# Kernel optimization log

Measured on AMD Instinct MI355X. Metric: run time of the kernel, lower is better.

## Reference

```python
import jax, jax.numpy as jnp
import numpy as np

B, T, D = 4, 2048, 1024  # batch, seq, latent_dim == attn_dim
H = 16                   # n_heads
HS = D // H              # head_size = 64
FF = 4 * D               # ffn hidden
EPS = 1e-5


def layernorm(x, g, b):
    mu = jnp.mean(x, axis=-1, keepdims=True)
    var = jnp.mean(jnp.square(x - mu), axis=-1, keepdims=True)
    return (x - mu) * jax.lax.rsqrt(var + EPS) * g + b


def setup_inputs() -> dict:
    key = jax.random.key(0)
    ks = jax.random.split(key, 12)
    s = lambda fan_in: 1.0 / np.sqrt(fan_in)
    return {
        "x": jax.random.normal(ks[0], (B, T, D), dtype=jnp.float32),
        "ln1_g": jnp.ones((D,), jnp.float32),
        "ln1_b": jnp.zeros((D,), jnp.float32),
        "W_ap": jax.random.normal(ks[1], (D, D), jnp.float32) * s(D),
        "b_ap": jnp.zeros((D,), jnp.float32),
        "W_qkv": jax.random.normal(ks[2], (D, 3 * D), jnp.float32) * s(D),
        "b_qkv": jnp.zeros((3 * D,), jnp.float32),
        "W_proj": jax.random.normal(ks[3], (D, D), jnp.float32) * s(D),
        "b_proj": jnp.zeros((D,), jnp.float32),
        "ln2_g": jnp.ones((D,), jnp.float32),
        "ln2_b": jnp.zeros((D,), jnp.float32),
        "W1": jax.random.normal(ks[4], (D, FF), jnp.float32) * s(D),
        "b1": jnp.zeros((FF,), jnp.float32),
        "W2": jax.random.normal(ks[5], (FF, D), jnp.float32) * s(FF),
        "b2": jnp.zeros((D,), jnp.float32),
    }


def block_fwd(x, ln1_g, ln1_b, W_ap, b_ap, W_qkv, b_qkv, W_proj, b_proj,
              ln2_g, ln2_b, W1, b1, W2, b2):
    # --- self attention branch ---
    a = layernorm(x, ln1_g, ln1_b)
    a = a @ W_ap + b_ap                       # [B,T,D]
    qkv = a @ W_qkv + b_qkv                   # [B,T,3D]
    q, k, v = jnp.split(qkv, 3, axis=-1)
    q = q.reshape(B, T, H, HS).transpose(0, 2, 1, 3)  # [B,H,T,HS]
    k = k.reshape(B, T, H, HS).transpose(0, 2, 1, 3)
    v = v.reshape(B, T, H, HS).transpose(0, 2, 1, 3)
    scores = jnp.einsum('bhqd,bhkd->bhqk', q, k) * (1.0 / np.sqrt(HS))
    probs = jax.nn.softmax(scores, axis=-1)   # full [B,H,T,T], no causal mask (as in source)
    o = jnp.einsum('bhqk,bhkd->bhqd', probs, v)
    o = o.transpose(0, 2, 1, 3).reshape(B, T, D)
    o = o @ W_proj + b_proj
    h = x + o
    # --- ffn branch: GELU(LayerNorm(h)) -> Linear -> GELU -> Linear ---
    f = jax.nn.gelu(layernorm(h, ln2_g, ln2_b), approximate=False)
    f = jax.nn.gelu(f @ W1 + b1, approximate=False) @ W2 + b2
    return h + f


def reference(x, ln1_g, ln1_b, W_ap, b_ap, W_qkv, b_qkv, W_proj, b_proj,
              ln2_g, ln2_b, W1, b1, W2, b2):
    return block_fwd(x, ln1_g, ln1_b, W_ap, b_ap, W_qkv, b_qkv, W_proj, b_proj,
                     ln2_g, ln2_b, W1, b1, W2, b2)
```

## Files before the change

kernel.cpp:

```cpp
#include <hip/hip_runtime.h>
#include <hip/hip_bf16.h>
#include <math.h>


typedef unsigned short u16;
typedef __attribute__((ext_vector_type(8))) short s16x8;
typedef __attribute__((ext_vector_type(4))) float f32x4;

__device__ __forceinline__ u16 f2bf(float f) {
    unsigned u = __float_as_uint(f);
    u += 0x7fffu + ((u >> 16) & 1u);
    return (u16)(u >> 16);
}
__device__ __forceinline__ unsigned pkbf2(float a, float b) {
    float2 t; t.x = a; t.y = b;
    __hip_bfloat162 r = __float22bfloat162_rn(t);
    return *(unsigned*)&r;
}
__device__ __forceinline__ float bf2f(short s) {
    return __uint_as_float(((unsigned)(unsigned short)s) << 16);
}
__device__ __forceinline__ float gelu_f(float v) {
    float u = v * v;
    float x = v * fmaf(0.0356774081f, u, 0.7978845608f);
    float t = __builtin_amdgcn_exp2f(x * 2.885390082f);
    float th = fmaf(-2.0f, __builtin_amdgcn_rcpf(t + 1.0f), 1.0f);
    float hv = 0.5f * v;
    return fmaf(hv, th, hv);
}
__device__ __forceinline__ void glds16(const u16* g, u16* l) {
    __builtin_amdgcn_global_load_lds(
        (const __attribute__((address_space(1))) void*)g,
        (__attribute__((address_space(3))) void*)l, 16, 0, 0);
}
__device__ __forceinline__ void barfence() {
    __builtin_amdgcn_s_barrier();
    asm volatile("" ::: "memory");
}

__global__ __launch_bounds__(256) void transpose_f32_bf16(
    const float* __restrict__ in, u16* __restrict__ out, int K, int N) {
    __shared__ float t[32][33];
    int n0 = blockIdx.x * 32, k0 = blockIdx.y * 32;
    int c = threadIdx.x, r0 = threadIdx.y;
#pragma unroll
    for (int i = 0; i < 4; i++) {
        int r = r0 + i * 8;
        t[r][c] = in[(size_t)(k0 + r) * N + n0 + c];
    }
    __syncthreads();
#pragma unroll
    for (int i = 0; i < 4; i++) {
        int r = r0 + i * 8;
        out[(size_t)(n0 + r) * K + k0 + c] = f2bf(t[c][r]);
    }
}

template <bool GELU>
__global__ __launch_bounds__(256) void ln_kernel(
    const float* __restrict__ x, const float* __restrict__ g,
    const float* __restrict__ bt, u16* __restrict__ out) {
    const int D = 1024;
    int row = blockIdx.x;
    float4 v = reinterpret_cast<const float4*>(x + (size_t)row * D)[threadIdx.x];
    float s = v.x + v.y + v.z + v.w;
    float s2 = v.x * v.x + v.y * v.y + v.z * v.z + v.w * v.w;
#pragma unroll
    for (int off = 32; off > 0; off >>= 1) {
        s += __shfl_down(s, off);
        s2 += __shfl_down(s2, off);
    }
    __shared__ float red[8];
    int wid = threadIdx.x >> 6;
    if ((threadIdx.x & 63) == 0) { red[wid] = s; red[wid + 4] = s2; }
    __syncthreads();
    s = red[0] + red[1] + red[2] + red[3];
    s2 = red[4] + red[5] + red[6] + red[7];
    float mu = s * (1.0f / 1024.0f);
    float var = s2 * (1.0f / 1024.0f) - mu * mu;
    float rstd = rsqrtf(var + 1e-5f);
    float4 gg = reinterpret_cast<const float4*>(g)[threadIdx.x];
    float4 bb = reinterpret_cast<const float4*>(bt)[threadIdx.x];
    float o0 = (v.x - mu) * rstd * gg.x + bb.x;
    float o1 = (v.y - mu) * rstd * gg.y + bb.y;
    float o2 = (v.z - mu) * rstd * gg.z + bb.z;
    float o3 = (v.w - mu) * rstd * gg.w + bb.w;
    if (GELU) { o0 = gelu_f(o0); o1 = gelu_f(o1); o2 = gelu_f(o2); o3 = gelu_f(o3); }
    uint2 o;
    o.x = pkbf2(o0, o1); o.y = pkbf2(o2, o3);
    reinterpret_cast<uint2*>(out + (size_t)row * D)[threadIdx.x] = o;
}

template <int OUT_BF16, int ACT_GELU, int HAS_RES, int SPLIT_V>
__global__ __launch_bounds__(512, 2) void gemm_kernel(
    const u16* __restrict__ A, const u16* __restrict__ BT,
    const float* __restrict__ bias, const float* __restrict__ res,
    void* __restrict__ outp, u16* __restrict__ vtg, int M, int N, int K) {
    __shared__ u16 As[2 * 256 * 64];
    __shared__ u16 Bs[2 * 256 * 64];
    const int nwg = gridDim.x * gridDim.y;
    int wg = blockIdx.y * gridDim.x + blockIdx.x;
    wg = (wg & 7) * (nwg >> 3) + (wg >> 3);
    const int m0 = (wg / gridDim.x) * 256, n0 = (wg % gridDim.x) * 256;
    const int tid = threadIdx.x;
    const int w = tid >> 6, lane = tid & 63, l16 = lane & 15, quad = lane >> 4;
    const int wm = w >> 2, wn = w & 3;

    const int lrow = lane >> 3;
    const int lcol = ((lane & 7) ^ lrow) * 8;
    const u16* Ag = A + (size_t)(m0 + w * 16 + lrow) * K + lcol;
    const u16* Bg = BT + (size_t)(n0 + w * 16 + lrow) * K + lcol;

    const int cx0 = (quad ^ (l16 & 7)) * 8;
    const int cx1 = cx0 ^ 32;

    f32x4 acc[2][2][4][2] = {};
    const int nt = K >> 6;

#define STAGE_A(AH, BUF, KK)                                              \
    do {                                                                  \
        const u16* _s = Ag + (size_t)((AH) * 128) * K + (KK);             \
        u16* _d = As + (BUF) * 16384 + ((AH) * 128 + w * 16) * 64;        \
        glds16(_s, _d);                                                   \
        glds16(_s + (size_t)8 * K, _d + 512);                             \
    } while (0)
#define STAGE_B(BH, BUF, KK)                                              \
    do {                                                                  \
        const u16* _s = Bg + (size_t)((BH) * 128) * K + (KK);             \
        u16* _d = Bs + (BUF) * 16384 + ((BH) * 128 + w * 16) * 64;        \
        glds16(_s, _d);                                                   \
        glds16(_s + (size_t)8 * K, _d + 512);                             \
    } while (0)

    STAGE_A(0, 0, 0);
    STAGE_B(0, 0, 0);
    STAGE_B(1, 0, 0);
    STAGE_A(1, 0, 0);
    asm volatile("s_waitcnt vmcnt(4)" ::: "memory");
    barfence();

    s16x8 af[4][2], bfA[2][2], bfB[2][2];

    for (int t = 0; t < nt; ++t) {
        const int cur = t & 1, nxt = cur ^ 1;
        const int kk = (t + 1) << 6;
        const bool pre = (t + 1) < nt;
        const u16* Ab = As + cur * 16384;
        const u16* Bb = Bs + cur * 16384;

#pragma unroll
        for (int i = 0; i < 4; ++i) {
            const u16* p = Ab + (wm * 64 + i * 16 + l16) * 64;
            af[i][0] = *(const s16x8*)(p + cx0);
            af[i][1] = *(const s16x8*)(p + cx1);
        }
#pragma unroll
        for (int j = 0; j < 2; ++j) {
            const u16* p = Bb + (wn * 32 + j * 16 + l16) * 64;
            bfA[j][0] = *(const s16x8*)(p + cx0);
            bfA[j][1] = *(const s16x8*)(p + cx1);
        }
        if (pre) STAGE_A(0, nxt, kk);
        barfence();
        asm volatile("s_waitcnt lgkmcnt(0)" ::: "memory");
        __builtin_amdgcn_sched_barrier(0);
        __builtin_amdgcn_s_setprio(1);
#pragma unroll
        for (int kd = 0; kd < 2; ++kd)
#pragma unroll
            for (int i = 0; i < 4; ++i)
#pragma unroll
                for (int j = 0; j < 2; ++j)
                    acc[0][0][i][j] = __builtin_amdgcn_mfma_f32_16x16x32_bf16(
                        af[i][kd], bfA[j][kd], acc[0][0][i][j], 0, 0, 0);
        __builtin_amdgcn_s_setprio(0);
        if (pre) asm volatile("s_waitcnt vmcnt(4)" ::: "memory");
        else     asm volatile("s_waitcnt vmcnt(2)" ::: "memory");
        barfence();

#pragma unroll
        for (int j = 0; j < 2; ++j) {
            const u16* p = Bb + (128 + wn * 32 + j * 16 + l16) * 64;
            bfB[j][0] = *(const s16x8*)(p + cx0);
            bfB[j][1] = *(const s16x8*)(p + cx1);
        }
        if (pre) STAGE_B(0, nxt, kk);
        barfence();
        asm volatile("s_waitcnt lgkmcnt(0)" ::: "memory");
        __builtin_amdgcn_sched_barrier(0);
        __builtin_amdgcn_s_setprio(1);
#pragma unroll
        for (int kd = 0; kd < 2; ++kd)
#pragma unroll
            for (int i = 0; i < 4; ++i)
#pragma unroll
                for (int j = 0; j < 2; ++j)
                    acc[0][1][i][j] = __builtin_amdgcn_mfma_f32_16x16x32_bf16(
                        af[i][kd], bfB[j][kd], acc[0][1][i][j], 0, 0, 0);
        __builtin_amdgcn_s_setprio(0);
        if (pre) asm volatile("s_waitcnt vmcnt(4)" ::: "memory");
        else     asm volatile("s_waitcnt vmcnt(0)" ::: "memory");
        barfence();

#pragma unroll
        for (int i = 0; i < 4; ++i) {
            const u16* p = Ab + (128 + wm * 64 + i * 16 + l16) * 64;
            af[i][0] = *(const s16x8*)(p + cx0);
            af[i][1] = *(const s16x8*)(p + cx1);
        }
        if (pre) STAGE_B(1, nxt, kk);
        barfence();
        asm volatile("s_waitcnt lgkmcnt(0)" ::: "memory");
        __builtin_amdgcn_sched_barrier(0);
        __builtin_amdgcn_s_setprio(1);
#pragma unroll
        for (int kd = 0; kd < 2; ++kd)
#pragma unroll
            for (int i = 0; i < 4; ++i)
#pragma unroll
                for (int j = 0; j < 2; ++j)
                    acc[1][1][i][j] = __builtin_amdgcn_mfma_f32_16x16x32_bf16(
                        af[i][kd], bfB[j][kd], acc[1][1][i][j], 0, 0, 0);
        __builtin_amdgcn_s_setprio(0);
        barfence();

        if (pre) STAGE_A(1, nxt, kk);
        __builtin_amdgcn_sched_barrier(0);
        __builtin_amdgcn_s_setprio(1);
#pragma unroll
        for (int kd = 0; kd < 2; ++kd)
#pragma unroll
            for (int i = 0; i < 4; ++i)
#pragma unroll
                for (int j = 0; j < 2; ++j)
                    acc[1][0][i][j] = __builtin_amdgcn_mfma_f32_16x16x32_bf16(
                        af[i][kd], bfA[j][kd], acc[1][0][i][j], 0, 0, 0);
        __builtin_amdgcn_s_setprio(0);
        if (pre) {
            asm volatile("s_waitcnt vmcnt(4)" ::: "memory");
            barfence();
        }
    }
#undef STAGE_A
#undef STAGE_B

    float bv[2][2];
#pragma unroll
    for (int bh = 0; bh < 2; ++bh)
#pragma unroll
        for (int j = 0; j < 2; ++j)
            bv[bh][j] = bias[n0 + bh * 128 + wn * 32 + j * 16 + l16];

    if (SPLIT_V && n0 >= 2048) {
#pragma unroll
        for (int ah = 0; ah < 2; ++ah)
#pragma unroll
            for (int i = 0; i < 4; ++i) {
                int rowb = m0 + ah * 128 + wm * 64 + i * 16 + quad * 4;
                int bb = rowb >> 11, tt = rowb & 2047;
#pragma unroll
                for (int bh = 0; bh < 2; ++bh)
#pragma unroll
                    for (int j = 0; j < 2; ++j) {
                        int vcol = n0 + bh * 128 + wn * 32 + j * 16 + l16 - 2048;
                        uint2 pk;
                        pk.x = pkbf2(acc[ah][bh][i][j][0] + bv[bh][j],
                                     acc[ah][bh][i][j][1] + bv[bh][j]);
                        pk.y = pkbf2(acc[ah][bh][i][j][2] + bv[bh][j],
                                     acc[ah][bh][i][j][3] + bv[bh][j]);
                        *(uint2*)&vtg[((size_t)bb * 1024 + vcol) * 2048 + tt] = pk;
                    }
            }
    } else {
#pragma unroll
        for (int ah = 0; ah < 2; ++ah)
#pragma unroll
            for (int i = 0; i < 4; ++i) {
                int rowb = m0 + ah * 128 + wm * 64 + i * 16 + quad * 4;
#pragma unroll
                for (int bh = 0; bh < 2; ++bh)
#pragma unroll
                    for (int j = 0; j < 2; ++j) {
                        int col = n0 + bh * 128 + wn * 32 + j * 16 + l16;
#pragma unroll
                        for (int r = 0; r < 4; ++r) {
                            float v = acc[ah][bh][i][j][r] + bv[bh][j];
                            if (ACT_GELU) v = gelu_f(v);
                            size_t idx = (size_t)(rowb + r) * N + col;
                            if (HAS_RES) v += res[idx];
                            if (OUT_BF16) ((u16*)outp)[idx] = f2bf(v);
                            else          ((float*)outp)[idx] = v;
                        }
                    }
            }
    }
}

template <int OUT_BF16, int HAS_RES>
__global__ __launch_bounds__(512, 2) void gemm_n128(
    const u16* __restrict__ A, const u16* __restrict__ BT,
    const float* __restrict__ bias, const float* __restrict__ res,
    void* __restrict__ outp, int M, int N, int K) {
    __shared__ u16 As[3 * 256 * 64];
    __shared__ u16 Bs[3 * 128 * 64];
    const int nwg = gridDim.x * gridDim.y;
    int wg = blockIdx.y * gridDim.x + blockIdx.x;
    wg = (wg & 7) * (nwg >> 3) + (wg >> 3);
    const int m0 = (wg / gridDim.x) * 256, n0 = (wg % gridDim.x) * 128;
    const int tid = threadIdx.x;
    const int w = tid >> 6, lane = tid & 63, l16 = lane & 15, quad = lane >> 4;
    const int wm = w >> 1, wn = w & 1;

    const int lrow = lane >> 3;
    const int lcol = ((lane & 7) ^ lrow) * 8;
    const u16* Ag = A + (size_t)(m0 + w * 16 + lrow) * K + lcol;
    const u16* Bg = BT + (size_t)(n0 + w * 16 + lrow) * K + lcol;

    const int cx0 = (quad ^ (l16 & 7)) * 8;
    const int cx1 = cx0 ^ 32;

    f32x4 acc[4][4] = {};
    const int nt = K >> 6;

#define NSTAGE_A(BUF, KK)                                                 \
    do {                                                                  \
        const u16* _s = Ag + (KK);                                        \
        u16* _d = As + (BUF) * 16384 + (w * 16) * 64;                     \
        glds16(_s, _d);                                                   \
        glds16(_s + (size_t)8 * K, _d + 512);                             \
        glds16(_s + (size_t)128 * K, _d + 8192);                          \
        glds16(_s + (size_t)136 * K, _d + 8192 + 512);                    \
    } while (0)
#define NSTAGE_B(BUF, KK)                                                 \
    do {                                                                  \
        const u16* _s = Bg + (KK);                                        \
        u16* _d = Bs + (BUF) * 8192 + (w * 16) * 64;                      \
        glds16(_s, _d);                                                   \
        glds16(_s + (size_t)8 * K, _d + 512);                             \
    } while (0)

    NSTAGE_A(0, 0);
    NSTAGE_B(0, 0);
    NSTAGE_A(1, 64);
    NSTAGE_B(1, 64);
    asm volatile("s_waitcnt vmcnt(6)" ::: "memory");
    barfence();

    s16x8 af[4][2], bf[2][2];
    int cur = 0, b2 = 2;
    for (int t = 0; t < nt; ++t) {
        const bool pre2 = (t + 2) < nt;
        const u16* Ab = As + cur * 16384;
        const u16* Bb = Bs + cur * 8192;
        const int kk2 = (t + 2) << 6;

#pragma unroll
        for (int i = 0; i < 4; ++i) {
            const u16* p = Ab + (wm * 64 + i * 16 + l16) * 64;
            af[i][0] = *(const s16x8*)(p + cx0);
            af[i][1] = *(const s16x8*)(p + cx1);
        }
#pragma unroll
        for (int j = 0; j < 2; ++j) {
            const u16* p = Bb + (wn * 64 + j * 16 + l16) * 64;
            bf[j][0] = *(const s16x8*)(p + cx0);
            bf[j][1] = *(const s16x8*)(p + cx1);
        }
        if (pre2) NSTAGE_A(b2, kk2);
        barfence();
        asm volatile("s_waitcnt lgkmcnt(0)" ::: "memory");
        __builtin_amdgcn_sched_barrier(0);
        __builtin_amdgcn_s_setprio(1);
#pragma unroll
        for (int kd = 0; kd < 2; ++kd)
#pragma unroll
            for (int i = 0; i < 4; ++i)
#pragma unroll
                for (int j = 0; j < 2; ++j)
                    acc[i][j] = __builtin_amdgcn_mfma_f32_16x16x32_bf16(
                        af[i][kd], bf[j][kd], acc[i][j], 0, 0, 0);
        __builtin_amdgcn_s_setprio(0);
        barfence();

#pragma unroll
        for (int j = 0; j < 2; ++j) {
            const u16* p = Bb + (wn * 64 + 32 + j * 16 + l16) * 64;
            bf[j][0] = *(const s16x8*)(p + cx0);
            bf[j][1] = *(const s16x8*)(p + cx1);
        }
        if (pre2) NSTAGE_B(b2, kk2);
        barfence();
        asm volatile("s_waitcnt lgkmcnt(0)" ::: "memory");
        __builtin_amdgcn_sched_barrier(0);
        __builtin_amdgcn_s_setprio(1);
#pragma unroll
        for (int kd = 0; kd < 2; ++kd)
#pragma unroll
            for (int i = 0; i < 4; ++i)
#pragma unroll
                for (int j = 0; j < 2; ++j)
                    acc[i][2 + j] = __builtin_amdgcn_mfma_f32_16x16x32_bf16(
                        af[i][kd], bf[j][kd], acc[i][2 + j], 0, 0, 0);
        __builtin_amdgcn_s_setprio(0);
        if (pre2)               asm volatile("s_waitcnt vmcnt(6)" ::: "memory");
        else if (t + 1 < nt)    asm volatile("s_waitcnt vmcnt(0)" ::: "memory");
        if (t + 1 < nt) barfence();

        cur = (cur == 2) ? 0 : cur + 1;
        b2 = (b2 == 2) ? 0 : b2 + 1;
    }
#undef NSTAGE_A
#undef NSTAGE_B

    float bv[4];
#pragma unroll
    for (int j = 0; j < 4; ++j) bv[j] = bias[n0 + wn * 64 + j * 16 + l16];

#pragma unroll
    for (int i = 0; i < 4; ++i) {
        int rowb = m0 + wm * 64 + i * 16 + quad * 4;
#pragma unroll
        for (int j = 0; j < 4; ++j) {
            int col = n0 + wn * 64 + j * 16 + l16;
#pragma unroll
            for (int r = 0; r < 4; ++r) {
                float v = acc[i][j][r] + bv[j];
                size_t idx = (size_t)(rowb + r) * N + col;
                if (HAS_RES) v += res[idx];
                if (OUT_BF16) ((u16*)outp)[idx] = f2bf(v);
                else          ((float*)outp)[idx] = v;
            }
        }
    }
}

__global__ __launch_bounds__(256) void knorm_kernel(
    const u16* __restrict__ qkv, float* __restrict__ maxkn) {
    const int T = 2048, D3 = 3072;
    int bh = blockIdx.x, b = bh >> 4, h = bh & 15;
    const u16* kg = qkv + (size_t)b * T * D3 + 1024 + h * 64;
    float mx = 0.f;
#pragma unroll
    for (int i = 0; i < 8; i++) {
        const u16* kp = kg + (size_t)(threadIdx.x + i * 256) * D3;
        float ss = 0.f;
#pragma unroll
        for (int c = 0; c < 8; c++) {
            s16x8 v = *(const s16x8*)(kp + c * 8);
#pragma unroll
            for (int j = 0; j < 8; j++) { float f = bf2f(v[j]); ss = fmaf(f, f, ss); }
        }
        mx = fmaxf(mx, ss);
    }
#pragma unroll
    for (int off = 32; off > 0; off >>= 1) mx = fmaxf(mx, __shfl_down(mx, off));
    __shared__ float red[4];
    if ((threadIdx.x & 63) == 0) red[threadIdx.x >> 6] = mx;
    __syncthreads();
    if (threadIdx.x == 0)
        maxkn[bh] = sqrtf(fmaxf(fmaxf(red[0], red[1]), fmaxf(red[2], red[3])));
}

__global__ __launch_bounds__(256, 4) void attn_kernel(
    const u16* __restrict__ qkv, const u16* __restrict__ vtg,
    const float* __restrict__ maxkn, u16* __restrict__ o) {
    const int T = 2048, D3 = 3072, Dm = 1024;
    const int bh = blockIdx.x, qb = blockIdx.y;
    const int b = bh >> 4, h = bh & 15;
    const int tid = threadIdx.x;
    const int w = tid >> 6, lane = tid & 63, l16 = lane & 15, quad = lane >> 4;
    const size_t tokbase = (size_t)b * T;
    const float s2 = 0.125f * 1.44269504088896f;

    __shared__ u16 Ks[64 * 72];
    __shared__ u16 Vts[64 * 72];
    __shared__ u16 Pt[4][32 * 72];

    s16x8 bq[2][2];
    float m2[2];
    const float kn = maxkn[bh];
#pragma unroll
    for (int qs = 0; qs < 2; qs++) {
        int qrow = qb * 128 + w * 32 + qs * 16 + l16;
        const u16* qp = qkv + (tokbase + qrow) * D3 + h * 64 + quad * 8;
        bq[qs][0] = *(const s16x8*)qp;
        bq[qs][1] = *(const s16x8*)(qp + 32);
        float ss = 0.f;
#pragma unroll
        for (int kd = 0; kd < 2; kd++)
#pragma unroll
            for (int j = 0; j < 8; j++) {
                float v = bf2f(bq[qs][kd][j]); ss = fmaf(v, v, ss);
            }
        ss += __shfl_xor(ss, 16);
        ss += __shfl_xor(ss, 32);
        m2[qs] = sqrtf(ss) * kn * s2;
    }

    f32x4 acc_ot[2][4] = {};
    float lp[2] = {0.f, 0.f};

    const u16* kgbase = qkv + tokbase * D3 + 1024 + h * 64;
    const u16* vgbase = vtg + ((size_t)b * 1024 + h * 64) * T;

    const int srow = tid >> 3;
    const int scv = (tid & 7) * 8;

    for (int kt = 0; kt < 32; kt++) {
        __syncthreads();
#pragma unroll
        for (int s = 0; s < 2; s++) {
            int row = srow + s * 32;
            *(s16x8*)&Ks[row * 72 + scv] =
                *(const s16x8*)(kgbase + (size_t)(kt * 64 + row) * D3 + scv);
            *(s16x8*)&Vts[row * 72 + scv] =
                *(const s16x8*)(vgbase + (size_t)row * T + kt * 64 + scv);
        }
        __syncthreads();

        f32x4 st[2][4] = {};
#pragma unroll
        for (int kd = 0; kd < 2; kd++)
#pragma unroll
            for (int kb = 0; kb < 4; kb++) {
                s16x8 ak = *(const s16x8*)&Ks[(kb * 16 + l16) * 72 + kd * 32 + quad * 8];
#pragma unroll
                for (int qs = 0; qs < 2; qs++)
                    st[qs][kb] = __builtin_amdgcn_mfma_f32_16x16x32_bf16(
                        ak, bq[qs][kd], st[qs][kb], 0, 0, 0);
            }

#pragma unroll
        for (int qs = 0; qs < 2; qs++) {
            float acc_l = 0.f;
#pragma unroll
            for (int kb = 0; kb < 4; kb++) {
#pragma unroll
                for (int r = 0; r < 4; r++) {
                    float pv = __builtin_amdgcn_exp2f(fmaf(st[qs][kb][r], s2, -m2[qs]));
                    st[qs][kb][r] = pv;
                    acc_l += pv;
                }
                uint2 pk;
                pk.x = pkbf2(st[qs][kb][0], st[qs][kb][1]);
                pk.y = pkbf2(st[qs][kb][2], st[qs][kb][3]);
                *(uint2*)&Pt[w][(qs * 16 + l16) * 72 + kb * 16 + quad * 4] = pk;
            }
            lp[qs] += acc_l;
        }

#pragma unroll
        for (int kk = 0; kk < 2; kk++) {
            s16x8 bp[2];
#pragma unroll
            for (int qs = 0; qs < 2; qs++)
                bp[qs] = *(const s16x8*)&Pt[w][(qs * 16 + l16) * 72 + kk * 32 + quad * 8];
#pragma unroll
            for (int dt = 0; dt < 4; dt++) {
                s16x8 av = *(const s16x8*)&Vts[(dt * 16 + l16) * 72 + kk * 32 + quad * 8];
#pragma unroll
                for (int qs = 0; qs < 2; qs++)
                    acc_ot[qs][dt] = __builtin_amdgcn_mfma_f32_16x16x32_bf16(
                        av, bp[qs], acc_ot[qs][dt], 0, 0, 0);
            }
        }
    }

#pragma unroll
    for (int qs = 0; qs < 2; qs++) {
        float l = lp[qs];
        l += __shfl_xor(l, 16);
        l += __shfl_xor(l, 32);
        float inv = 1.0f / l;
        int token = qb * 128 + w * 32 + qs * 16 + l16;
#pragma unroll
        for (int dt = 0; dt < 4; dt++) {
            uint2 pk;
            pk.x = pkbf2(acc_ot[qs][dt][0] * inv, acc_ot[qs][dt][1] * inv);
            pk.y = pkbf2(acc_ot[qs][dt][2] * inv, acc_ot[qs][dt][3] * inv);
            *(uint2*)&o[(tokbase + token) * Dm + h * 64 + dt * 16 + quad * 4] = pk;
        }
    }
}

extern "C" void kernel_launch(void* const* d_in, const int* in_sizes, int n_in,
                              void* d_out, int out_size, void* d_ws, size_t ws_size,
                              hipStream_t stream) {
    const int M = 8192;
    const int D = 1024, D3 = 3072, FF = 4096;

    const float* x      = (const float*)d_in[0];
    const float* ln1_g  = (const float*)d_in[1];
    const float* ln1_b  = (const float*)d_in[2];
    const float* W_ap   = (const float*)d_in[3];
    const float* b_ap   = (const float*)d_in[4];
    const float* W_qkv  = (const float*)d_in[5];
    const float* b_qkv  = (const float*)d_in[6];
    const float* W_proj = (const float*)d_in[7];
    const float* b_proj = (const float*)d_in[8];
    const float* ln2_g  = (const float*)d_in[9];
    const float* ln2_b  = (const float*)d_in[10];
    const float* W1     = (const float*)d_in[11];
    const float* b1     = (const float*)d_in[12];
    const float* W2     = (const float*)d_in[13];
    const float* b2     = (const float*)d_in[14];

    char* p = (char*)d_ws;
    auto carve = [&](size_t bytes) { char* r = p; p += (bytes + 255) & ~(size_t)255; return r; };
    u16*   WapT   = (u16*)carve((size_t)D * D * 2);
    u16*   WqkvT  = (u16*)carve((size_t)D * D3 * 2);
    u16*   WprojT = (u16*)carve((size_t)D * D * 2);
    u16*   W1T    = (u16*)carve((size_t)D * FF * 2);
    u16*   W2T    = (u16*)carve((size_t)FF * D * 2);
    u16*   aln    = (u16*)carve((size_t)M * D * 2);
    u16*   a1     = (u16*)carve((size_t)M * D * 2);
    u16*   qkvb   = (u16*)carve((size_t)M * D3 * 2);
    float* hbuf   = (float*)carve((size_t)M * D * 4);
    u16*   f1     = (u16*)carve((size_t)M * FF * 2);
    float* maxkn  = (float*)carve(64 * 4);
    u16* gbuf = aln;
    u16* obuf = a1;
    u16* vtg  = f1;

    dim3 tb(32, 8);
    transpose_f32_bf16<<<dim3(D / 32, D / 32), tb, 0, stream>>>(W_ap, WapT, D, D);
    transpose_f32_bf16<<<dim3(D3 / 32, D / 32), tb, 0, stream>>>(W_qkv, WqkvT, D, D3);
    transpose_f32_bf16<<<dim3(D / 32, D / 32), tb, 0, stream>>>(W_proj, WprojT, D, D);
    transpose_f32_bf16<<<dim3(FF / 32, D / 32), tb, 0, stream>>>(W1, W1T, D, FF);
    transpose_f32_bf16<<<dim3(D / 32, FF / 32), tb, 0, stream>>>(W2, W2T, FF, D);

    ln_kernel<false><<<M, 256, 0, stream>>>(x, ln1_g, ln1_b, aln);
    gemm_n128<1, 0><<<dim3(D / 128, M / 256), 512, 0, stream>>>(
        aln, WapT, b_ap, nullptr, a1, M, D, D);
    gemm_kernel<1, 0, 0, 1><<<dim3(D3 / 256, M / 256), 512, 0, stream>>>(
        a1, WqkvT, b_qkv, nullptr, qkvb, vtg, M, D3, D);
    knorm_kernel<<<64, 256, 0, stream>>>(qkvb, maxkn);
    attn_kernel<<<dim3(64, 16), 256, 0, stream>>>(qkvb, vtg, maxkn, obuf);
    gemm_n128<0, 1><<<dim3(D / 128, M / 256), 512, 0, stream>>>(
        obuf, WprojT, b_proj, x, hbuf, M, D, D);
    ln_kernel<true><<<M, 256, 0, stream>>>(hbuf, ln2_g, ln2_b, gbuf);
    gemm_kernel<1, 1, 0, 0><<<dim3(FF / 256, M / 256), 512, 0, stream>>>(
        gbuf, W1T, b1, nullptr, f1, nullptr, M, FF, D);
    gemm_n128<0, 1><<<dim3(D / 128, M / 256), 512, 0, stream>>>(
        f1, W2T, b2, hbuf, (float*)d_out, M, D, FF);
}
```

Before: 539.1 us.

## Double-buffer attention K/V tiles with async LDS loads and swizzled layout

The attention kernel now stages K and V^T tiles into two LDS buffers with direct global-to-LDS loads. The next tile is prefetched while the current one is computed, which replaces the two syncthreads per iteration with one wait and a fence. Shared layouts drop the padding to 64 columns and use an XOR swizzle, and the MFMA sections get raised scheduling priority. Occupancy hint drops to 3 blocks per CU to fit the larger LDS footprint. The QKV projection also moves from the 256-wide GEMM to the 128-wide three-stage GEMM, with the V-transpose epilogue carried over.

Result: no change. 543.7 us (+0.9%).

```diff
diff --git a/kernel.cpp b/kernel.cpp
--- a/kernel.cpp
+++ b/kernel.cpp
@@ -91,11 +91,11 @@
     reinterpret_cast<uint2*>(out + (size_t)row * D)[threadIdx.x] = o;
 }
 
-template <int OUT_BF16, int ACT_GELU, int HAS_RES, int SPLIT_V>
+template <int OUT_BF16, int ACT_GELU, int HAS_RES>
 __global__ __launch_bounds__(512, 2) void gemm_kernel(
     const u16* __restrict__ A, const u16* __restrict__ BT,
     const float* __restrict__ bias, const float* __restrict__ res,
-    void* __restrict__ outp, u16* __restrict__ vtg, int M, int N, int K) {
+    void* __restrict__ outp, int M, int N, int K) {
     __shared__ u16 As[2 * 256 * 64];
     __shared__ u16 Bs[2 * 256 * 64];
     const int nwg = gridDim.x * gridDim.y;
@@ -251,56 +251,34 @@
         for (int j = 0; j < 2; ++j)
             bv[bh][j] = bias[n0 + bh * 128 + wn * 32 + j * 16 + l16];
 
-    if (SPLIT_V && n0 >= 2048) {
-#pragma unroll
-        for (int ah = 0; ah < 2; ++ah)
-#pragma unroll
-            for (int i = 0; i < 4; ++i) {
-                int rowb = m0 + ah * 128 + wm * 64 + i * 16 + quad * 4;
-                int bb = rowb >> 11, tt = rowb & 2047;
-#pragma unroll
-                for (int bh = 0; bh < 2; ++bh)
-#pragma unroll
-                    for (int j = 0; j < 2; ++j) {
-                        int vcol = n0 + bh * 128 + wn * 32 + j * 16 + l16 - 2048;
-                        uint2 pk;
-                        pk.x = pkbf2(acc[ah][bh][i][j][0] + bv[bh][j],
-                                     acc[ah][bh][i][j][1] + bv[bh][j]);
-                        pk.y = pkbf2(acc[ah][bh][i][j][2] + bv[bh][j],
-                                     acc[ah][bh][i][j][3] + bv[bh][j]);
-                        *(uint2*)&vtg[((size_t)bb * 1024 + vcol) * 2048 + tt] = pk;
+#pragma unroll
+    for (int ah = 0; ah < 2; ++ah)
+#pragma unroll
+        for (int i = 0; i < 4; ++i) {
+            int rowb = m0 + ah * 128 + wm * 64 + i * 16 + quad * 4;
+#pragma unroll
+            for (int bh = 0; bh < 2; ++bh)
+#pragma unroll
+                for (int j = 0; j < 2; ++j) {
+                    int col = n0 + bh * 128 + wn * 32 + j * 16 + l16;
+#pragma unroll
+                    for (int r = 0; r < 4; ++r) {
+                        float v = acc[ah][bh][i][j][r] + bv[bh][j];
+                        if (ACT_GELU) v = gelu_f(v);
+                        size_t idx = (size_t)(rowb + r) * N + col;
+                        if (HAS_RES) v += res[idx];
+                        if (OUT_BF16) ((u16*)outp)[idx] = f2bf(v);
+                        else          ((float*)outp)[idx] = v;
                     }
-            }
-    } else {
-#pragma unroll
-        for (int ah = 0; ah < 2; ++ah)
-#pragma unroll
-            for (int i = 0; i < 4; ++i) {
-                int rowb = m0 + ah * 128 + wm * 64 + i * 16 + quad * 4;
-#pragma unroll
-                for (int bh = 0; bh < 2; ++bh)
-#pragma unroll
-                    for (int j = 0; j < 2; ++j) {
-                        int col = n0 + bh * 128 + wn * 32 + j * 16 + l16;
-#pragma unroll
-                        for (int r = 0; r < 4; ++r) {
-                            float v = acc[ah][bh][i][j][r] + bv[bh][j];
-                            if (ACT_GELU) v = gelu_f(v);
-                            size_t idx = (size_t)(rowb + r) * N + col;
-                            if (HAS_RES) v += res[idx];
-                            if (OUT_BF16) ((u16*)outp)[idx] = f2bf(v);
-                            else          ((float*)outp)[idx] = v;
-                        }
-                    }
-            }
-    }
-}
-
-template <int OUT_BF16, int HAS_RES>
+                }
+        }
+}
+
+template <int OUT_BF16, int HAS_RES, int SPLIT_V>
 __global__ __launch_bounds__(512, 2) void gemm_n128(
     const u16* __restrict__ A, const u16* __restrict__ BT,
     const float* __restrict__ bias, const float* __restrict__ res,
-    void* __restrict__ outp, int M, int N, int K) {
+    void* __restrict__ outp, u16* __restrict__ vtg, int M, int N, int K) {
     __shared__ u16 As[3 * 256 * 64];
     __shared__ u16 Bs[3 * 128 * 64];
     const int nwg = gridDim.x * gridDim.y;
@@ -416,19 +394,35 @@
 #pragma unroll
     for (int j = 0; j < 4; ++j) bv[j] = bias[n0 + wn * 64 + j * 16 + l16];
 
-#pragma unroll
-    for (int i = 0; i < 4; ++i) {
-        int rowb = m0 + wm * 64 + i * 16 + quad * 4;
-#pragma unroll
-        for (int j = 0; j < 4; ++j) {
-            int col = n0 + wn * 64 + j * 16 + l16;
-#pragma unroll
-            for (int r = 0; r < 4; ++r) {
-                float v = acc[i][j][r] + bv[j];
-                size_t idx = (size_t)(rowb + r) * N + col;
-                if (HAS_RES) v += res[idx];
-                if (OUT_BF16) ((u16*)outp)[idx] = f2bf(v);
-                else          ((float*)outp)[idx] = v;
+    if (SPLIT_V && n0 >= 2048) {
+#pragma unroll
+        for (int i = 0; i < 4; ++i) {
+            int rowb = m0 + wm * 64 + i * 16 + quad * 4;
+            int bb = rowb >> 11, tt = rowb & 2047;
+#pragma unroll
+            for (int j = 0; j < 4; ++j) {
+                int vcol = n0 + wn * 64 + j * 16 + l16 - 2048;
+                uint2 pk;
+                pk.x = pkbf2(acc[i][j][0] + bv[j], acc[i][j][1] + bv[j]);
+                pk.y = pkbf2(acc[i][j][2] + bv[j], acc[i][j][3] + bv[j]);
+                *(uint2*)&vtg[((size_t)bb * 1024 + vcol) * 2048 + tt] = pk;
+            }
+        }
+    } else {
+#pragma unroll
+        for (int i = 0; i < 4; ++i) {
+            int rowb = m0 + wm * 64 + i * 16 + quad * 4;
+#pragma unroll
+            for (int j = 0; j < 4; ++j) {
+                int col = n0 + wn * 64 + j * 16 + l16;
+#pragma unroll
+                for (int r = 0; r < 4; ++r) {
+                    float v = acc[i][j][r] + bv[j];
+                    size_t idx = (size_t)(rowb + r) * N + col;
+                    if (HAS_RES) v += res[idx];
+                    if (OUT_BF16) ((u16*)outp)[idx] = f2bf(v);
+                    else          ((float*)outp)[idx] = v;
+                }
             }
         }
     }
@@ -461,7 +455,7 @@
         maxkn[bh] = sqrtf(fmaxf(fmaxf(red[0], red[1]), fmaxf(red[2], red[3])));
 }
 
-__global__ __launch_bounds__(256, 4) void attn_kernel(
+__global__ __launch_bounds__(256, 3) void attn_kernel(
     const u16* __restrict__ qkv, const u16* __restrict__ vtg,
     const float* __restrict__ maxkn, u16* __restrict__ o) {
     const int T = 2048, D3 = 3072, Dm = 1024;
@@ -472,9 +466,9 @@
     const size_t tokbase = (size_t)b * T;
     const float s2 = 0.125f * 1.44269504088896f;
 
-    __shared__ u16 Ks[64 * 72];
-    __shared__ u16 Vts[64 * 72];
-    __shared__ u16 Pt[4][32 * 72];
+    __shared__ u16 Ks[2][64 * 64];
+    __shared__ u16 Vts[2][64 * 64];
+    __shared__ u16 Pt[4][32 * 64];
 
     s16x8 bq[2][2];
     float m2[2];
@@ -500,39 +494,50 @@
     f32x4 acc_ot[2][4] = {};
     float lp[2] = {0.f, 0.f};
 
-    const u16* kgbase = qkv + tokbase * D3 + 1024 + h * 64;
-    const u16* vgbase = vtg + ((size_t)b * 1024 + h * 64) * T;
-
-    const int srow = tid >> 3;
-    const int scv = (tid & 7) * 8;
+    const int lr = lane >> 3;
+    const int lcs = ((lane & 7) ^ lr) * 8;
+    const u16* kgl = qkv + tokbase * D3 + 1024 + h * 64 + (size_t)(w * 16 + lr) * D3 + lcs;
+    const u16* vgl = vtg + ((size_t)b * 1024 + h * 64 + w * 16 + lr) * T + lcs;
+
+    const int cq0 = (quad ^ (l16 & 7)) * 8;
+    const int cq1 = cq0 ^ 32;
+
+#define ASTAGE(BUF, KT)                                                   \
+    do {                                                                  \
+        const u16* _k = kgl + (size_t)(KT) * 64 * D3;                     \
+        glds16(_k, &Ks[BUF][(w * 16) * 64]);                              \
+        glds16(_k + (size_t)8 * D3, &Ks[BUF][(w * 16 + 8) * 64]);         \
+        const u16* _v = vgl + (KT) * 64;                                  \
+        glds16(_v, &Vts[BUF][(w * 16) * 64]);                             \
+        glds16(_v + (size_t)8 * T, &Vts[BUF][(w * 16 + 8) * 64]);         \
+    } while (0)
+
+    ASTAGE(0, 0);
+    asm volatile("s_waitcnt vmcnt(0)" ::: "memory");
+    barfence();
 
     for (int kt = 0; kt < 32; kt++) {
-        __syncthreads();
-#pragma unroll
-        for (int s = 0; s < 2; s++) {
-            int row = srow + s * 32;
-            *(s16x8*)&Ks[row * 72 + scv] =
-                *(const s16x8*)(kgbase + (size_t)(kt * 64 + row) * D3 + scv);
-            *(s16x8*)&Vts[row * 72 + scv] =
-                *(const s16x8*)(vgbase + (size_t)row * T + kt * 64 + scv);
-        }
-        __syncthreads();
+        const int cur = kt & 1;
+        if (kt + 1 < 32) ASTAGE(cur ^ 1, kt + 1);
 
         f32x4 st[2][4] = {};
+        __builtin_amdgcn_s_setprio(1);
 #pragma unroll
         for (int kd = 0; kd < 2; kd++)
 #pragma unroll
             for (int kb = 0; kb < 4; kb++) {
-                s16x8 ak = *(const s16x8*)&Ks[(kb * 16 + l16) * 72 + kd * 32 + quad * 8];
+                s16x8 ak = *(const s16x8*)&Ks[cur][(kb * 16 + l16) * 64 + (kd ? cq1 : cq0)];
 #pragma unroll
                 for (int qs = 0; qs < 2; qs++)
                     st[qs][kb] = __builtin_amdgcn_mfma_f32_16x16x32_bf16(
                         ak, bq[qs][kd], st[qs][kb], 0, 0, 0);
             }
+        __builtin_amdgcn_s_setprio(0);
 
 #pragma unroll
         for (int qs = 0; qs < 2; qs++) {
             float acc_l = 0.f;
+            const int prow = (qs * 16 + l16) * 64;
 #pragma unroll
             for (int kb = 0; kb < 4; kb++) {
 #pragma unroll
@@ -544,7 +549,8 @@
                 uint2 pk;
                 pk.x = pkbf2(st[qs][kb][0], st[qs][kb][1]);
                 pk.y = pkbf2(st[qs][kb][2], st[qs][kb][3]);
-                *(uint2*)&Pt[w][(qs * 16 + l16) * 72 + kb * 16 + quad * 4] = pk;
+                int slot = ((kb * 2 + (quad >> 1)) ^ (l16 & 7)) * 8 + (quad & 1) * 4;
+                *(uint2*)&Pt[w][prow + slot] = pk;
             }
             lp[qs] += acc_l;
         }
@@ -554,17 +560,23 @@
             s16x8 bp[2];
 #pragma unroll
             for (int qs = 0; qs < 2; qs++)
-                bp[qs] = *(const s16x8*)&Pt[w][(qs * 16 + l16) * 72 + kk * 32 + quad * 8];
+                bp[qs] = *(const s16x8*)&Pt[w][(qs * 16 + l16) * 64 + (kk ? cq1 : cq0)];
+            __builtin_amdgcn_s_setprio(1);
 #pragma unroll
             for (int dt = 0; dt < 4; dt++) {
-                s16x8 av = *(const s16x8*)&Vts[(dt * 16 + l16) * 72 + kk * 32 + quad * 8];
+                s16x8 av = *(const s16x8*)&Vts[cur][(dt * 16 + l16) * 64 + (kk ? cq1 : cq0)];
 #pragma unroll
                 for (int qs = 0; qs < 2; qs++)
                     acc_ot[qs][dt] = __builtin_amdgcn_mfma_f32_16x16x32_bf16(
                         av, bp[qs], acc_ot[qs][dt], 0, 0, 0);
             }
-        }
-    }
+            __builtin_amdgcn_s_setprio(0);
+        }
+
+        if (kt + 1 < 32) asm volatile("s_waitcnt vmcnt(0)" ::: "memory");
+        barfence();
+    }
+#undef ASTAGE
 
 #pragma unroll
     for (int qs = 0; qs < 2; qs++) {
@@ -630,17 +642,17 @@
     transpose_f32_bf16<<<dim3(D / 32, FF / 32), tb, 0, stream>>>(W2, W2T, FF, D);
 
     ln_kernel<false><<<M, 256, 0, stream>>>(x, ln1_g, ln1_b, aln);
-    gemm_n128<1, 0><<<dim3(D / 128, M / 256), 512, 0, stream>>>(
-        aln, WapT, b_ap, nullptr, a1, M, D, D);
-    gemm_kernel<1, 0, 0, 1><<<dim3(D3 / 256, M / 256), 512, 0, stream>>>(
+    gemm_n128<1, 0, 0><<<dim3(D / 128, M / 256), 512, 0, stream>>>(
+        aln, WapT, b_ap, nullptr, a1, nullptr, M, D, D);
+    gemm_n128<1, 0, 1><<<dim3(D3 / 128, M / 256), 512, 0, stream>>>(
         a1, WqkvT, b_qkv, nullptr, qkvb, vtg, M, D3, D);
     knorm_kernel<<<64, 256, 0, stream>>>(qkvb, maxkn);
     attn_kernel<<<dim3(64, 16), 256, 0, stream>>>(qkvb, vtg, maxkn, obuf);
-    gemm_n128<0, 1><<<dim3(D / 128, M / 256), 512, 0, stream>>>(
-        obuf, WprojT, b_proj, x, hbuf, M, D, D);
+    gemm_n128<0, 1, 0><<<dim3(D / 128, M / 256), 512, 0, stream>>>(
+        obuf, WprojT, b_proj, x, hbuf, nullptr, M, D, D);
     ln_kernel<true><<<M, 256, 0, stream>>>(hbuf, ln2_g, ln2_b, gbuf);
-    gemm_kernel<1, 1, 0, 0><<<dim3(FF / 256, M / 256), 512, 0, stream>>>(
-        gbuf, W1T, b1, nullptr, f1, nullptr, M, FF, D);
-    gemm_n128<0, 1><<<dim3(D / 128, M / 256), 512, 0, stream>>>(
-        f1, W2T, b2, hbuf, (float*)d_out, M, D, FF);
-}
+    gemm_kernel<1, 1, 0><<<dim3(FF / 256, M / 256), 512, 0, stream>>>(
+        gbuf, W1T, b1, nullptr, f1, M, FF, D);
+    gemm_n128<0, 1, 0><<<dim3(D / 128, M / 256), 512, 0, stream>>>(
+        f1, W2T, b2, hbuf, (float*)d_out, nullptr, M, D, FF);
+}
```
